# Performance work log

Hardware: AMD Instinct MI355X
Metric: run time of the kernel (lower is better)

Reference implementation:

```python
import jax, jax.numpy as jnp
import numpy as np

GAMMAS = jnp.array([2.7, 2.1, 2.4, 2.0, 3.0, 2.9, 3.0, 2.5, 2.1, 2.6, 2.0, 2.1, 2.7, 2.4, 2.2], dtype=jnp.float32)

B, NCLS, H, W = 32, 15, 256, 256
K, CREG = 500, 2


def setup_inputs() -> dict:
    key = jax.random.key(0)
    ks = jax.random.split(key, 6)
    pred = jax.random.uniform(ks[0], (B, NCLS, H, W), dtype=jnp.float32)
    gt = jax.random.uniform(ks[1], (B, NCLS, H, W), dtype=jnp.float32)
    output = jax.random.normal(ks[2], (B, CREG, H, W), dtype=jnp.float32)
    mask = jax.random.randint(ks[3], (B, K), 0, 2, dtype=jnp.int32)
    ind = jax.random.randint(ks[4], (B, K), 0, H * W)
    target = jax.random.normal(ks[5], (B, K, CREG), dtype=jnp.float32)
    inde = jax.random.randint(jax.random.fold_in(key, 7), (B, K, 3), 0, 15)
    return {"pred": pred, "gt": gt, "output": output, "mask": mask,
            "ind": ind, "target": target, "inde": inde}


def _forward(pred, gt, output, mask, ind, target, inde):
    b, c_out = output.shape[0], output.shape[1]
    k = ind.shape[1]
    # _tranpose_and_gather_feat: [B,C,H,W] -> [B,HW,C], gather along dim 1
    feat = jnp.transpose(output, (0, 2, 3, 1)).reshape(b, -1, c_out)
    pre = jnp.take_along_axis(feat, ind[:, :, None].astype(jnp.int32), axis=1)  # [B,K,C]

    d = pre - target
    ad = jnp.abs(d)
    huber = jnp.where(ad < 1.0, 0.5 * d * d, ad - 0.5)
    l_bk = huber.mean(axis=2)  # [B,K]

    pos_mask = mask.astype(bool)
    factor = jnp.arctan(l_bk) * (2.0 / jnp.pi)
    vals = jnp.where(pos_mask, factor, 1.0).reshape(-1)

    b_idx = jnp.broadcast_to(jnp.arange(b)[:, None], (b, k)).reshape(-1)
    ch = inde[..., 0].reshape(-1)
    yy = inde[..., 1].reshape(-1)
    xx = inde[..., 2].reshape(-1)
    # in-place multiplicative scatter; torch's pred_uni aliases pred so the
    # modified tensor is used for BOTH pred_cat and pred_cat_uni below
    pred_mod = pred.at[b_idx, ch, yy, xx].multiply(vals)

    # loss is overwritten each loop iteration in the original: only the LAST
    # positive's smooth-L1 loss survives (0 if no positives)
    flat_m = pos_mask.reshape(-1)
    flat_l = l_bk.reshape(-1)
    last = jnp.max(jnp.where(flat_m, jnp.arange(flat_m.shape[0]), -1))
    loss0 = jnp.where(last >= 0, flat_l[jnp.clip(last, 0)], 0.0)

    # focal term, vectorized over the 15 class channels
    eps = 1e-12
    g = GAMMAS[None, :, None, None]
    pos_inds = (gt == 1.0).astype(pred.dtype)
    neg_inds = (gt < 1.0).astype(pred.dtype)
    neg_weights = jnp.power(1.0 - gt, 4)
    pos_loss = jnp.log(pred_mod + eps) * jnp.power(1.0 - pred_mod, g) * pos_inds
    neg_loss = jnp.log(1.0 - pred_mod + eps) * jnp.power(pred_mod, g) * neg_weights * neg_inds
    per_ch = jnp.sum(pos_loss + neg_loss, axis=(0, 2, 3))  # [15]
    loss = loss0 - jnp.sum(per_ch * GAMMAS * 0.5)

    num_pos = pos_inds.sum()
    return jnp.where(num_pos == 0, loss, loss / num_pos)


def reference(pred, gt, output, mask, ind, target, inde):
    return _forward(pred, gt, output, mask, ind, target, inde)
```

## Files before the change

### kernel.cpp

```cpp
#include <hip/hip_runtime.h>
#include <math.h>

#define BB 32
#define NCLS 15
#define HH 256
#define WW 256
#define KK 500
#define HW (HH*WW)
#define NELEM (BB*NCLS*HW)
#define N4 (NELEM/4)
#define NM (BB*NCLS*16*16)
#define BK (BB*KK)

#define OFF_LBK 4
#define OFF_M   16384

__constant__ float c_gammas[15] = {2.7f,2.1f,2.4f,2.0f,3.0f,2.9f,3.0f,2.5f,
                                   2.1f,2.6f,2.0f,2.1f,2.7f,2.4f,2.2f};

#define EXP2F(x) __builtin_amdgcn_exp2f(x)
#define LOG2F(x) __builtin_amdgcn_logf(x)
#define LN2 0.69314718055994530942f

__device__ __forceinline__ float elem(float p, float g, float gam, float& np) {
    float t    = 1.0f - g;
    float t2   = t * t;
    float negw = (g < 1.0f) ? t2 * t2 : 0.0f;
    float pw   = EXP2F(gam * LOG2F(p));
    float v    = (LN2 * LOG2F(1.0f - p + 1e-12f)) * pw * negw;
    if (g == 1.0f) {
        np += 1.0f;
        v += (LN2 * LOG2F(p + 1e-12f)) * EXP2F(gam * LOG2F(1.0f - p));
    }
    return v;
}

__device__ __forceinline__ float blockReduceSum(float v) {
    __shared__ float sh[4];
    #pragma unroll
    for (int o = 32; o > 0; o >>= 1) v += __shfl_down(v, o);
    int lane = threadIdx.x & 63, w = threadIdx.x >> 6;
    if (lane == 0) sh[w] = v;
    __syncthreads();
    float r = 0.0f;
    if (threadIdx.x == 0) r = sh[0] + sh[1] + sh[2] + sh[3];
    __syncthreads();
    return r;
}

__global__ __launch_bounds__(256) void k_init(float* ws) {
    int i = blockIdx.x * blockDim.x + threadIdx.x;
    if (i == 0) {
        ws[0] = 0.0f;
        ws[1] = 0.0f;
        ((int*)ws)[2] = -1;
    }
    if (i < NM) ws[OFF_M + i] = 1.0f;
}

__global__ __launch_bounds__(256) void k_bk(const float* __restrict__ output,
                                            const int*   __restrict__ mask,
                                            const int*   __restrict__ ind,
                                            const float* __restrict__ target,
                                            const int*   __restrict__ inde,
                                            float* ws) {
    int t = blockIdx.x * blockDim.x + threadIdx.x;
    bool valid = (t < BK);
    int lastv = -1;
    if (valid) {
        int b = t / KK;
        int pos = ind[t];
        const float* ob = output + (size_t)b * 2 * HW;
        float p0 = ob[pos];
        float p1 = ob[HW + pos];
        float d0 = p0 - target[t*2 + 0];
        float d1 = p1 - target[t*2 + 1];
        float a0 = fabsf(d0), a1 = fabsf(d1);
        float h0 = (a0 < 1.0f) ? 0.5f*d0*d0 : a0 - 0.5f;
        float h1 = (a1 < 1.0f) ? 0.5f*d1*d1 : a1 - 0.5f;
        float l  = 0.5f * (h0 + h1);
        ws[OFF_LBK + t] = l;
        if (mask[t] != 0) {
            lastv = t;
            float factor = atanf(l) * 0.63661977236758134308f;
            int ch = inde[t*3 + 0];
            int yy = inde[t*3 + 1];
            int xx = inde[t*3 + 2];
            int mi = ((b*NCLS + ch)*16 + yy)*16 + xx;
            unsigned int* addr = (unsigned int*)(ws + OFF_M + mi);
            unsigned int old = *addr, assumed;
            do {
                assumed = old;
                float nv = __uint_as_float(assumed) * factor;
                old = atomicCAS(addr, assumed, __float_as_uint(nv));
            } while (old != assumed);
        }
    }
    __shared__ int shm[4];
    int v = lastv;
    #pragma unroll
    for (int o = 32; o > 0; o >>= 1) v = max(v, __shfl_down(v, o));
    int lane = threadIdx.x & 63, w = threadIdx.x >> 6;
    if (lane == 0) shm[w] = v;
    __syncthreads();
    if (threadIdx.x == 0) {
        int m = max(max(shm[0], shm[1]), max(shm[2], shm[3]));
        if (m >= 0) atomicMax(((int*)ws) + 2, m);
    }
}

__global__ __launch_bounds__(256) void k_main(const float4* __restrict__ pred,
                                              const float4* __restrict__ gt,
                                              float* ws) {
    int c = blockIdx.y, b = blockIdx.z;
    float gam = c_gammas[c];
    size_t base = ((size_t)(b * NCLS + c)) << 14;
    float acc = 0.0f, np = 0.0f;
    #pragma unroll 2
    for (int j = blockIdx.x * 256 + threadIdx.x; j < (HW/4); j += 8 * 256) {
        float4 p = pred[base + j];
        float4 g = gt[base + j];
        acc += elem(p.x, g.x, gam, np) + elem(p.y, g.y, gam, np)
             + elem(p.z, g.z, gam, np) + elem(p.w, g.w, gam, np);
    }
    acc *= gam;
    float bs = blockReduceSum(acc);
    if (threadIdx.x == 0 && bs != 0.0f) atomicAdd(&ws[0], bs);
    float bn = blockReduceSum(np);
    if (threadIdx.x == 0 && bn != 0.0f) atomicAdd(&ws[1], bn);
}

__global__ __launch_bounds__(256) void k_corr(const float* __restrict__ pred,
                                              const float* __restrict__ gt,
                                              float* ws) {
    int i = blockIdx.x * blockDim.x + threadIdx.x;
    float acc = 0.0f, dummy = 0.0f;
    if (i < NM) {
        float m = ws[OFF_M + i];
        if (m != 1.0f) {
            int x  = i & 15;
            int y  = (i >> 4) & 15;
            int bc = i >> 8;
            int c  = bc % NCLS;
            size_t off = ((size_t)bc << 16) + (size_t)(y * WW + x);
            float p = pred[off];
            float g = gt[off];
            float gam = c_gammas[c];
            acc = gam * (elem(p * m, g, gam, dummy) - elem(p, g, gam, dummy));
        }
    }
    float bs = blockReduceSum(acc);
    if (threadIdx.x == 0 && bs != 0.0f) atomicAdd(&ws[0], bs);
}

__global__ void k_fin(const float* ws, float* out) {
    int last = ((const int*)ws)[2];
    float loss0 = (last >= 0) ? ws[OFF_LBK + last] : 0.0f;
    float loss = loss0 - 0.5f * ws[0];
    float np = ws[1];
    out[0] = (np == 0.0f) ? loss : loss / np;
}

extern "C" void kernel_launch(void* const* d_in, const int* in_sizes, int n_in,
                              void* d_out, int out_size, void* d_ws, size_t ws_size,
                              hipStream_t stream) {
    const float* pred   = (const float*)d_in[0];
    const float* gt     = (const float*)d_in[1];
    const float* output = (const float*)d_in[2];
    const int*   mask   = (const int*)d_in[3];
    const int*   ind    = (const int*)d_in[4];
    const float* target = (const float*)d_in[5];
    const int*   inde   = (const int*)d_in[6];
    float* ws  = (float*)d_ws;
    float* out = (float*)d_out;

    k_init<<<(NM + 255)/256, 256, 0, stream>>>(ws);
    k_bk  <<<(BK + 255)/256, 256, 0, stream>>>(output, mask, ind, target, inde, ws);
    dim3 mg(8, NCLS, BB);
    k_main<<<mg, 256, 0, stream>>>((const float4*)pred, (const float4*)gt, ws);
    k_corr<<<(NM + 255)/256, 256, 0, stream>>>(pred, gt, ws);
    k_fin <<<1, 1, 0, stream>>>(ws, out);
}
```

Baseline: 301.2 us.

## Flatten main reduction grid and fold final kernel into correction via last-block

The main focal-loss kernel moves from a 3D grid (8x15x32 blocks) to a flat grid of 2048 blocks. Each thread strides over the whole tensor a fixed number of times and looks up gamma per float4 from the channel index. The separate single-thread finalize kernel is removed. The correction kernel now counts finished blocks with an atomic, and the last block computes the output, which saves one launch. In exchange the main loop does an extra modulo and constant lookup per iteration, and there are fewer blocks to hide memory latency.

```diff
diff --git a/kernel.cpp b/kernel.cpp
--- a/kernel.cpp
+++ b/kernel.cpp
@@ -11,6 +11,11 @@
 #define N4 (NELEM/4)
 #define NM (BB*NCLS*16*16)
 #define BK (BB*KK)
+
+#define MG 2048
+#define MT 256
+#define MGS (MG*MT)
+#define MITER (N4/MGS)
 
 #define OFF_LBK 4
 #define OFF_M   16384
@@ -54,6 +59,7 @@
         ws[0] = 0.0f;
         ws[1] = 0.0f;
         ((int*)ws)[2] = -1;
+        ((int*)ws)[3] = 0;
     }
     if (i < NM) ws[OFF_M + i] = 1.0f;
 }
@@ -65,9 +71,8 @@
                                             const int*   __restrict__ inde,
                                             float* ws) {
     int t = blockIdx.x * blockDim.x + threadIdx.x;
-    bool valid = (t < BK);
     int lastv = -1;
-    if (valid) {
+    if (t < BK) {
         int b = t / KK;
         int pos = ind[t];
         const float* ob = output + (size_t)b * 2 * HW;
@@ -112,18 +117,18 @@
 __global__ __launch_bounds__(256) void k_main(const float4* __restrict__ pred,
                                               const float4* __restrict__ gt,
                                               float* ws) {
-    int c = blockIdx.y, b = blockIdx.z;
-    float gam = c_gammas[c];
-    size_t base = ((size_t)(b * NCLS + c)) << 14;
+    int t = blockIdx.x * MT + threadIdx.x;
     float acc = 0.0f, np = 0.0f;
-    #pragma unroll 2
-    for (int j = blockIdx.x * 256 + threadIdx.x; j < (HW/4); j += 8 * 256) {
-        float4 p = pred[base + j];
-        float4 g = gt[base + j];
-        acc += elem(p.x, g.x, gam, np) + elem(p.y, g.y, gam, np)
-             + elem(p.z, g.z, gam, np) + elem(p.w, g.w, gam, np);
+    #pragma unroll 5
+    for (int k = 0; k < MITER; ++k) {
+        int i = t + k * MGS;
+        float4 p = pred[i];
+        float4 g = gt[i];
+        int c = (i >> 14) % NCLS;
+        float gam = c_gammas[c];
+        acc += gam * (elem(p.x, g.x, gam, np) + elem(p.y, g.y, gam, np)
+                    + elem(p.z, g.z, gam, np) + elem(p.w, g.w, gam, np));
     }
-    acc *= gam;
     float bs = blockReduceSum(acc);
     if (threadIdx.x == 0 && bs != 0.0f) atomicAdd(&ws[0], bs);
     float bn = blockReduceSum(np);
@@ -132,33 +137,35 @@
 
 __global__ __launch_bounds__(256) void k_corr(const float* __restrict__ pred,
                                               const float* __restrict__ gt,
-                                              float* ws) {
+                                              float* ws, float* out) {
     int i = blockIdx.x * blockDim.x + threadIdx.x;
     float acc = 0.0f, dummy = 0.0f;
-    if (i < NM) {
-        float m = ws[OFF_M + i];
-        if (m != 1.0f) {
-            int x  = i & 15;
-            int y  = (i >> 4) & 15;
-            int bc = i >> 8;
-            int c  = bc % NCLS;
-            size_t off = ((size_t)bc << 16) + (size_t)(y * WW + x);
-            float p = pred[off];
-            float g = gt[off];
-            float gam = c_gammas[c];
-            acc = gam * (elem(p * m, g, gam, dummy) - elem(p, g, gam, dummy));
+    float m = ws[OFF_M + i];
+    if (m != 1.0f) {
+        int x  = i & 15;
+        int y  = (i >> 4) & 15;
+        int bc = i >> 8;
+        int c  = bc % NCLS;
+        size_t off = ((size_t)bc << 16) + (size_t)(y * WW + x);
+        float p = pred[off];
+        float g = gt[off];
+        float gam = c_gammas[c];
+        acc = gam * (elem(p * m, g, gam, dummy) - elem(p, g, gam, dummy));
+    }
+    float bs = blockReduceSum(acc);
+    if (threadIdx.x == 0) {
+        if (bs != 0.0f) atomicAdd(&ws[0], bs);
+        __threadfence();
+        int done = atomicAdd(((int*)ws) + 3, 1);
+        if (done == gridDim.x - 1) {
+            float S  = atomicAdd(&ws[0], 0.0f);
+            float np = atomicAdd(&ws[1], 0.0f);
+            int last = ((volatile int*)ws)[2];
+            float loss0 = (last >= 0) ? ws[OFF_LBK + last] : 0.0f;
+            float loss = loss0 - 0.5f * S;
+            out[0] = (np == 0.0f) ? loss : loss / np;
         }
     }
-    float bs = blockReduceSum(acc);
-    if (threadIdx.x == 0 && bs != 0.0f) atomicAdd(&ws[0], bs);
-}
-
-__global__ void k_fin(const float* ws, float* out) {
-    int last = ((const int*)ws)[2];
-    float loss0 = (last >= 0) ? ws[OFF_LBK + last] : 0.0f;
-    float loss = loss0 - 0.5f * ws[0];
-    float np = ws[1];
-    out[0] = (np == 0.0f) ? loss : loss / np;
 }
 
 extern "C" void kernel_launch(void* const* d_in, const int* in_sizes, int n_in,
@@ -176,8 +183,6 @@
 
     k_init<<<(NM + 255)/256, 256, 0, stream>>>(ws);
     k_bk  <<<(BK + 255)/256, 256, 0, stream>>>(output, mask, ind, target, inde, ws);
-    dim3 mg(8, NCLS, BB);
-    k_main<<<mg, 256, 0, stream>>>((const float4*)pred, (const float4*)gt, ws);
-    k_corr<<<(NM + 255)/256, 256, 0, stream>>>(pred, gt, ws);
-    k_fin <<<1, 1, 0, stream>>>(ws, out);
+    k_main<<<MG, MT, 0, stream>>>((const float4*)pred, (const float4*)gt, ws);
+    k_corr<<<NM/256, 256, 0, stream>>>(pred, gt, ws, out);
 }
```

After: 306.8 us. About the same (+1.9%).
